# Optimization experiments

Hardware: AMD Instinct MI355X
Metric: run time of the kernel (lower is better)

## Reference

```python
import jax, jax.numpy as jnp
import numpy as np

P = 4            # input_pooling
THR = 1.0        # snntorch Leaky default threshold
LI_THR = 1.0e5   # li threshold (never fires)
SLOPE = 50.0     # fast_sigmoid surrogate slope
BETA1 = min(0.999, 0.95)  # tau_mem_1, clamped as in forward
BETA2 = min(0.999, 0.9)   # tau_mem_2, clamped as in forward

@jax.custom_vjp
def spike(v):
    # heaviside forward, fast_sigmoid surrogate backward
    return (v > 0).astype(v.dtype)

def _spike_fwd(v):
    return (v > 0).astype(v.dtype), v

def _spike_bwd(v, g):
    return (g / (SLOPE * jnp.abs(v) + 1.0) ** 2,)

spike.defvjp(_spike_fwd, _spike_bwd)


def setup_inputs() -> dict:
    key = jax.random.key(0)
    k1, k2, k3 = jax.random.split(key, 3)
    B, T, H, W = 64, 100, 128, 128
    F = (H // P) * (W // P)  # 1024 = linear1 in-features
    x = jax.random.normal(k1, (B, T, H, W), jnp.float32)
    # torch Linear default init: U(-1/sqrt(fan_in), 1/sqrt(fan_in)), bias=False
    W1 = jax.random.uniform(k2, (200, F), jnp.float32, -1.0, 1.0) / np.sqrt(F).astype(np.float32)
    W2 = jax.random.uniform(k3, (1, 200), jnp.float32, -1.0, 1.0) / np.sqrt(200.0).astype(np.float32)
    return {"x": x, "W1": W1, "W2": W2}


def reference(x, W1, W2):
    B, T, H, W = x.shape
    # AvgPool2d(P): exact non-overlapping average pooling (H,W divisible by P)
    xp = x.reshape(B, T, H // P, P, W // P, P).mean(axis=(3, 5))
    g1 = jnp.einsum('btf,of->bto', xp.reshape(B, T, -1), W1)  # [B,T,200]

    def lif_step(mem, g):
        # snntorch Leaky (reset_mechanism='subtract', reset detached)
        reset = jax.lax.stop_gradient((mem > THR).astype(g.dtype))
        mem_n = BETA1 * mem + g - reset * THR
        z = spike(mem_n - THR)
        return mem_n, z

    _, zs = jax.lax.scan(lif_step, jnp.zeros((B, 200), x.dtype), jnp.swapaxes(g1, 0, 1))  # zs: [T,B,200]

    g2 = jnp.einsum('tbh,oh->tbo', zs, W2)  # [T,B,1]

    def li_step(mem, g):
        reset = jax.lax.stop_gradient((mem > LI_THR).astype(g.dtype))
        mem_n = BETA2 * mem + g - reset * LI_THR
        return mem_n, mem_n

    _, ys = jax.lax.scan(li_step, jnp.zeros((B, 1), x.dtype), g2)  # [T,B,1]
    return jnp.swapaxes(ys, 0, 1)  # y: [B,T,1]
```

## Files before the change

kernel.cpp:

```cpp
#include <hip/hip_runtime.h>
#include <hip/hip_bf16.h>

#define PB   64
#define PT   100
#define PH   128
#define PW   128
#define PF   1024
#define PM   (PB*PT)
#define PK   PF
#define PN   200
#define BETA1 0.95f
#define BETA2 0.9f

__global__ __launch_bounds__(256) void pool_kernel(const float* __restrict__ x,
                                                   float* __restrict__ xp) {
    const long total = (long)PM * PF;
    for (long idx = (long)blockIdx.x * blockDim.x + threadIdx.x; idx < total;
         idx += (long)gridDim.x * blockDim.x) {
        int f  = (int)(idx & (PF - 1));
        long bt = idx >> 10;
        int ph = f >> 5, pw = f & 31;
        const float* base = x + (bt * PH + ph * 4) * PW + pw * 4;
        float s = 0.0f;
#pragma unroll
        for (int i = 0; i < 4; ++i) {
            float4 v = *reinterpret_cast<const float4*>(base + i * PW);
            s += v.x + v.y + v.z + v.w;
        }
        xp[idx] = s * 0.0625f;
    }
}

#define BM 64
#define BN 64
#define BK 64
#define LPAD 4
__global__ __launch_bounds__(256) void gemm_kernel(const float* __restrict__ A,
                                                   const float* __restrict__ W1,
                                                   float* __restrict__ C) {
    __shared__ float Asl[BK][BM + LPAD];
    __shared__ float Wsl[BK][BN + LPAD];
    const int tid = threadIdx.x;
    const int m0 = (blockIdx.x >> 2) * BM;
    const int n0 = (blockIdx.x & 3) * BN;
    const int tn = tid & 15;
    const int tm = tid >> 4;
    const int lr  = tid >> 2;
    const int lc4 = (tid & 3) * 4;

    float acc[4][4] = {};

    for (int k0 = 0; k0 < PK; k0 += BK) {
#pragma unroll
        for (int p = 0; p < 4; ++p) {
            int kk = lc4 + p * 16;
            float4 v = *reinterpret_cast<const float4*>(
                &A[(long)(m0 + lr) * PK + k0 + kk]);
            Asl[kk + 0][lr] = v.x; Asl[kk + 1][lr] = v.y;
            Asl[kk + 2][lr] = v.z; Asl[kk + 3][lr] = v.w;
        }
#pragma unroll
        for (int p = 0; p < 4; ++p) {
            int kk = lc4 + p * 16;
            int row = n0 + lr;
            float4 v = make_float4(0.f, 0.f, 0.f, 0.f);
            if (row < PN)
                v = *reinterpret_cast<const float4*>(&W1[(long)row * PK + k0 + kk]);
            Wsl[kk + 0][lr] = v.x; Wsl[kk + 1][lr] = v.y;
            Wsl[kk + 2][lr] = v.z; Wsl[kk + 3][lr] = v.w;
        }
        __syncthreads();
#pragma unroll
        for (int k = 0; k < BK; ++k) {
            float4 av = *reinterpret_cast<const float4*>(&Asl[k][tm * 4]);
            float4 wv = *reinterpret_cast<const float4*>(&Wsl[k][tn * 4]);
            float a_[4] = {av.x, av.y, av.z, av.w};
            float w_[4] = {wv.x, wv.y, wv.z, wv.w};
#pragma unroll
            for (int i = 0; i < 4; ++i)
#pragma unroll
                for (int j = 0; j < 4; ++j)
                    acc[i][j] += a_[i] * w_[j];
        }
        __syncthreads();
    }
#pragma unroll
    for (int i = 0; i < 4; ++i) {
        int m = m0 + tm * 4 + i;
        int n = n0 + tn * 4;
        if (n < PN) {
            float4 v = make_float4(acc[i][0], acc[i][1], acc[i][2], acc[i][3]);
            *reinterpret_cast<float4*>(&C[(long)m * PN + n]) = v;
        }
    }
}

__global__ __launch_bounds__(256) void scan_kernel(const float* __restrict__ g1,
                                                   const float* __restrict__ W2,
                                                   float* __restrict__ y) {
    __shared__ float part[PT][4];
    const int b = blockIdx.x;
    const int o = threadIdx.x;
    const int wv = o >> 6;
    const int lane = o & 63;
    const float w2 = (o < PN) ? W2[o] : 0.0f;
    float mem = 0.0f;
    const float* gb = g1 + (long)b * PT * PN;

    for (int t = 0; t < PT; ++t) {
        float g = (o < PN) ? gb[t * PN + o] : 0.0f;
        float reset = (mem > 1.0f) ? 1.0f : 0.0f;
        mem = BETA1 * mem + g - reset;
        float c = ((mem - 1.0f) > 0.0f) ? w2 : 0.0f;
#pragma unroll
        for (int off = 32; off; off >>= 1)
            c += __shfl_xor(c, off, 64);
        if (lane == 0) part[t][wv] = c;
    }
    __syncthreads();
    if (o == 0) {
        float li = 0.0f;
        for (int t = 0; t < PT; ++t) {
            float g2 = part[t][0] + part[t][1] + part[t][2] + part[t][3];
            li = BETA2 * li + g2;
            y[b * PT + t] = li;
        }
    }
}

extern "C" void kernel_launch(void* const* d_in, const int* in_sizes, int n_in,
                              void* d_out, int out_size, void* d_ws, size_t ws_size,
                              hipStream_t stream) {
    const float* x  = (const float*)d_in[0];
    const float* W1 = (const float*)d_in[1];
    const float* W2 = (const float*)d_in[2];
    float* y = (float*)d_out;

    float* xp = (float*)d_ws;
    float* g1 = xp + (long)PM * PF;

    pool_kernel<<<2048, 256, 0, stream>>>(x, xp);
    gemm_kernel<<<(PM / BM) * 4, 256, 0, stream>>>(xp, W1, g1);
    scan_kernel<<<PB, 256, 0, stream>>>(g1, W2, y);
}
```

Measured before the change: 655.2 us.

## Fuse average pooling into GEMM A-tile load with XCD-aware block remap

Removes the separate pooling kernel and its intermediate buffer. The GEMM now computes each pooled A element directly from x while filling shared memory. The block index is remapped so that the four N-tiles of the same M-tile run on the same XCD, which aims to let the repeated reads of x be served from shared L2. In exchange, x is re-read once per N-tile, and the per-thread loads are strided across 16 rows, which may coalesce poorly.

```diff
diff --git a/kernel.cpp b/kernel.cpp
--- a/kernel.cpp
+++ b/kernel.cpp
@@ -12,52 +12,44 @@
 #define BETA1 0.95f
 #define BETA2 0.9f
 
-__global__ __launch_bounds__(256) void pool_kernel(const float* __restrict__ x,
-                                                   float* __restrict__ xp) {
-    const long total = (long)PM * PF;
-    for (long idx = (long)blockIdx.x * blockDim.x + threadIdx.x; idx < total;
-         idx += (long)gridDim.x * blockDim.x) {
-        int f  = (int)(idx & (PF - 1));
-        long bt = idx >> 10;
-        int ph = f >> 5, pw = f & 31;
-        const float* base = x + (bt * PH + ph * 4) * PW + pw * 4;
-        float s = 0.0f;
-#pragma unroll
-        for (int i = 0; i < 4; ++i) {
-            float4 v = *reinterpret_cast<const float4*>(base + i * PW);
-            s += v.x + v.y + v.z + v.w;
-        }
-        xp[idx] = s * 0.0625f;
-    }
-}
-
 #define BM 64
 #define BN 64
 #define BK 64
 #define LPAD 4
-__global__ __launch_bounds__(256) void gemm_kernel(const float* __restrict__ A,
-                                                   const float* __restrict__ W1,
-                                                   float* __restrict__ C) {
+__global__ __launch_bounds__(256) void fusedpool_gemm_kernel(const float* __restrict__ x,
+                                                             const float* __restrict__ W1,
+                                                             float* __restrict__ C) {
     __shared__ float Asl[BK][BM + LPAD];
     __shared__ float Wsl[BK][BN + LPAD];
     const int tid = threadIdx.x;
-    const int m0 = (blockIdx.x >> 2) * BM;
-    const int n0 = (blockIdx.x & 3) * BN;
+
+    const int rank = (blockIdx.x & 7) * 50 + (blockIdx.x >> 3);
+    const int m0 = (rank >> 2) * BM;
+    const int n0 = (rank & 3) * BN;
+
     const int tn = tid & 15;
     const int tm = tid >> 4;
     const int lr  = tid >> 2;
     const int lc4 = (tid & 3) * 4;
+    const int prow = tid >> 2;
+    const int q    = tid & 3;
 
+    const long rowbase = (long)(m0 + prow) * (PH * PW);
     float acc[4][4] = {};
 
     for (int k0 = 0; k0 < PK; k0 += BK) {
 #pragma unroll
-        for (int p = 0; p < 4; ++p) {
-            int kk = lc4 + p * 16;
-            float4 v = *reinterpret_cast<const float4*>(
-                &A[(long)(m0 + lr) * PK + k0 + kk]);
-            Asl[kk + 0][lr] = v.x; Asl[kk + 1][lr] = v.y;
-            Asl[kk + 2][lr] = v.z; Asl[kk + 3][lr] = v.w;
+        for (int j = 0; j < 16; ++j) {
+            int f  = k0 + q * 16 + j;
+            int ph = f >> 5, pw = f & 31;
+            const float* b0 = x + rowbase + ph * (4 * PW) + pw * 4;
+            float s = 0.0f;
+#pragma unroll
+            for (int i = 0; i < 4; ++i) {
+                float4 v = *reinterpret_cast<const float4*>(b0 + i * PW);
+                s += v.x + v.y + v.z + v.w;
+            }
+            Asl[q * 16 + j][prow] = s * 0.0625f;
         }
 #pragma unroll
         for (int p = 0; p < 4; ++p) {
@@ -136,10 +128,8 @@
     const float* W2 = (const float*)d_in[2];
     float* y = (float*)d_out;
 
-    float* xp = (float*)d_ws;
-    float* g1 = xp + (long)PM * PF;
+    float* g1 = (float*)d_ws;
 
-    pool_kernel<<<2048, 256, 0, stream>>>(x, xp);
-    gemm_kernel<<<(PM / BM) * 4, 256, 0, stream>>>(xp, W1, g1);
+    fusedpool_gemm_kernel<<<(PM / BM) * 4, 256, 0, stream>>>(x, W1, g1);
     scan_kernel<<<PB, 256, 0, stream>>>(g1, W2, y);
 }
```

Result: slower. 801.3 us (+22.3%).
